# Kernel tuning notes

Hardware: AMD Instinct MI355X
Metric: run time of the kernel (lower is better)

The kernel has to match this reference:

```python
import jax, jax.numpy as jnp
import numpy as np

# Quantum kernel closed form:
#   Encoder applies RY(x_k) on wire k from |0>, then RY(-y_k); RY(-y)RY(x) = RY(x-y).
#   Amplitude of |0...0> = prod_k <0|RY(x_k - y_k)|0> = prod_k cos((x_k - y_k)/2).
#   kernel(x, y) = | prod_k cos((x_k - y_k)/2) |.
# Using cos(a-b) = cos a cos b + sin a sin b avoids forming explicit pairwise diffs twice.

def setup_inputs() -> dict:
    key = jax.random.key(0)
    x = jax.random.normal(key, (32, 1024, 4), dtype=jnp.float32)  # [B, S, n_wires]
    return {"x": x}


def reference(x) -> jnp.ndarray:
    c = jnp.cos(0.5 * x)  # [B, S, W]
    s = jnp.sin(0.5 * x)
    # cos((x_i,k - x_j,k)/2) for all pairs -> [B, S, S, W]
    term = c[:, :, None, :] * c[:, None, :, :] + s[:, :, None, :] * s[:, None, :, :]
    kernel_mat = jnp.abs(jnp.prod(term, axis=-1))  # [B, S, S]
    attn = jax.nn.softmax(kernel_mat, axis=-1)
    return jnp.matmul(attn, x)  # [B, S, W]
```

## Files before the change

### kernel.cpp

```cpp
#include <hip/hip_runtime.h>


typedef _Float16 f16x8 __attribute__((ext_vector_type(8)));
typedef float    f32x16 __attribute__((ext_vector_type(16)));
typedef unsigned int u32x4 __attribute__((ext_vector_type(4)));

#define SQ 1024
#define NTHREADS 256
#define ROWS 32

__device__ __forceinline__ unsigned pk16(float a, float b) {
    auto p = __builtin_amdgcn_cvt_pkrtz(a, b);
    return __builtin_bit_cast(unsigned, p);
}

#if __has_builtin(__builtin_amdgcn_permlane32_swap)
__device__ __forceinline__ void pl32swap(unsigned &a, unsigned &b) {
    auto r = __builtin_amdgcn_permlane32_swap(a, b, false, false);
    a = r[0]; b = r[1];
}
#else
__device__ __forceinline__ void pl32swap(unsigned &a, unsigned &b) {
    asm("v_permlane32_swap_b32 %0, %1" : "+v"(a), "+v"(b));
}
#endif

__global__ __launch_bounds__(NTHREADS, 3)
void qka_kernel(const float* __restrict__ x, float* __restrict__ out) {
    __shared__ f16x8 lds_F0[SQ];
    __shared__ f16x8 lds_F1[SQ];
    __shared__ f16x8 lds_XT[5 * 129];

    const int bid   = blockIdx.x;
    const int b     = bid >> 5;
    const int Ibase = (bid & 31) * ROWS;
    const int tid   = threadIdx.x;

    const float4* xb  = (const float4*)(x + (size_t)b * SQ * 4);
    _Float16*     xtp = (_Float16*)lds_XT;

    #pragma unroll
    for (int k = 0; k < SQ / NTHREADS; ++k) {
        int j = tid + k * NTHREADS;
        float4 v = xb[j];
        float c0 = __cosf(0.5f * v.x), s0 = __sinf(0.5f * v.x);
        float c1 = __cosf(0.5f * v.y), s1 = __sinf(0.5f * v.y);
        float c2 = __cosf(0.5f * v.z), s2 = __sinf(0.5f * v.z);
        float c3 = __cosf(0.5f * v.w), s3 = __sinf(0.5f * v.w);
        float m0 = c0 * c1, m1 = s0 * c1, m2 = c0 * s1, m3 = s0 * s1;
        float n0 = m0 * c2, n1 = m1 * c2, n2 = m2 * c2, n3 = m3 * c2;
        float n4 = m0 * s2, n5 = m1 * s2, n6 = m2 * s2, n7 = m3 * s2;
        f16x8 p0, p1;
        p0[0] = (_Float16)(n0 * c3); p0[1] = (_Float16)(n1 * c3);
        p0[2] = (_Float16)(n2 * c3); p0[3] = (_Float16)(n3 * c3);
        p0[4] = (_Float16)(n4 * c3); p0[5] = (_Float16)(n5 * c3);
        p0[6] = (_Float16)(n6 * c3); p0[7] = (_Float16)(n7 * c3);
        p1[0] = (_Float16)(n0 * s3); p1[1] = (_Float16)(n1 * s3);
        p1[2] = (_Float16)(n2 * s3); p1[3] = (_Float16)(n3 * s3);
        p1[4] = (_Float16)(n4 * s3); p1[5] = (_Float16)(n5 * s3);
        p1[6] = (_Float16)(n6 * s3); p1[7] = (_Float16)(n7 * s3);
        int sj = j ^ ((j >> 3) & 7);
        lds_F0[sj] = p0;
        lds_F1[sj] = p1;
        xtp[0 * 1032 + j] = (_Float16)v.x;
        xtp[1 * 1032 + j] = (_Float16)v.y;
        xtp[2 * 1032 + j] = (_Float16)v.z;
        xtp[3 * 1032 + j] = (_Float16)v.w;
        xtp[4 * 1032 + j] = (_Float16)1.0f;
    }
    __syncthreads();

    const int wid  = tid >> 6;
    const int lane = tid & 63;
    const int h    = lane >> 5;
    const int ln   = lane & 31;

    const f16x8* Fh = h ? lds_F1 : lds_F0;
    int ib = Ibase + ln; ib ^= (ib >> 3) & 7;
    const f16x8 bfrag = Fh[ib];

    const int rowsel = (ln < 4) ? ln : 4;
    const int xbase  = rowsel * 129 + wid * 32 + h;

    f32x16 oacc = (f32x16)(0.0f);

    #pragma unroll 2
    for (int t = 0; t < 8; ++t) {
        int ja = wid * 256 + t * 32 + ln;
        ja ^= (ja >> 3) & 7;
        f16x8 afrag = Fh[ja];
        f32x16 d = __builtin_amdgcn_mfma_f32_32x32x16_f16(
            afrag, bfrag, (f32x16)(0.0f), 0, 0, 0);
        unsigned q0 = pk16(__expf(fabsf(d[0])),  __expf(fabsf(d[1])));
        unsigned q1 = pk16(__expf(fabsf(d[2])),  __expf(fabsf(d[3])));
        unsigned q2 = pk16(__expf(fabsf(d[4])),  __expf(fabsf(d[5])));
        unsigned q3 = pk16(__expf(fabsf(d[6])),  __expf(fabsf(d[7])));
        unsigned q4 = pk16(__expf(fabsf(d[8])),  __expf(fabsf(d[9])));
        unsigned q5 = pk16(__expf(fabsf(d[10])), __expf(fabsf(d[11])));
        unsigned q6 = pk16(__expf(fabsf(d[12])), __expf(fabsf(d[13])));
        unsigned q7 = pk16(__expf(fabsf(d[14])), __expf(fabsf(d[15])));
        pl32swap(q0, q2); pl32swap(q1, q3);
        pl32swap(q4, q6); pl32swap(q5, q7);
        u32x4 w0 = {q0, q1, q2, q3};
        u32x4 w1 = {q4, q5, q6, q7};
        f16x8 ef0 = __builtin_bit_cast(f16x8, w0);
        f16x8 ef1 = __builtin_bit_cast(f16x8, w1);
        f16x8 xf0 = lds_XT[xbase + t * 4];
        f16x8 xf1 = lds_XT[xbase + t * 4 + 2];
        oacc = __builtin_amdgcn_mfma_f32_32x32x16_f16(ef0, xf0, oacc, 0, 0, 0);
        oacc = __builtin_amdgcn_mfma_f32_32x32x16_f16(ef1, xf1, oacc, 0, 0, 0);
    }

    __syncthreads();
    float* ps = (float*)lds_F0;
    if (ln < 5) {
        #pragma unroll
        for (int r = 0; r < 16; ++r) {
            int m = (r & 3) + 8 * (r >> 2) + 4 * h;
            ps[(wid * 32 + m) * 8 + ln] = oacc[r];
        }
    }
    __syncthreads();

    if (tid < 32) {
        float nx = 0.f, ny = 0.f, nz = 0.f, nw = 0.f, den = 0.f;
        #pragma unroll
        for (int ww = 0; ww < 4; ++ww) {
            const float* p = &ps[(ww * 32 + tid) * 8];
            nx += p[0]; ny += p[1]; nz += p[2]; nw += p[3]; den += p[4];
        }
        float inv = 1.0f / den;
        ((float4*)out)[(size_t)b * SQ + Ibase + tid] =
            make_float4(nx * inv, ny * inv, nz * inv, nw * inv);
    }
}

extern "C" void kernel_launch(void* const* d_in, const int* in_sizes, int n_in,
                              void* d_out, int out_size, void* d_ws, size_t ws_size,
                              hipStream_t stream) {
    const float* x = (const float*)d_in[0];
    float* out = (float*)d_out;
    dim3 grid(32 * (SQ / ROWS));
    dim3 block(NTHREADS);
    qka_kernel<<<grid, block, 0, stream>>>(x, out);
}
```

Baseline: 13.47 us.

## Double rows per block, software-pipeline score MFMA, use exp2 with prescaled features

Each block now has 512 threads and handles 64 query rows, with two row tiles sharing one LDS feature table. This halves the number of blocks and the redundant per-batch trig and LDS setup. The score MFMA for the next tile is issued before the exp/pack of the current one, and the output accumulation is split into two independent accumulators to shorten MFMA dependency chains. The exp is replaced by a raw exp2 builtin, with the log2(e) scale folded into one feature factor. This relies on |sqrt(log2 e)^2 · d| equalling |d|·log2 e, and the larger scale factor adds a little fp16 rounding.

```diff
diff --git a/kernel.cpp b/kernel.cpp
--- a/kernel.cpp
+++ b/kernel.cpp
@@ -6,8 +6,8 @@
 typedef unsigned int u32x4 __attribute__((ext_vector_type(4)));
 
 #define SQ 1024
-#define NTHREADS 256
-#define ROWS 32
+#define NTHREADS 512
+#define ROWS 64
 
 __device__ __forceinline__ unsigned pk16(float a, float b) {
     auto p = __builtin_amdgcn_cvt_pkrtz(a, b);
@@ -25,15 +25,19 @@
 }
 #endif
 
-__global__ __launch_bounds__(NTHREADS, 3)
+__device__ __forceinline__ float ex2(float v) {
+    return __builtin_amdgcn_exp2f(fabsf(v));
+}
+
+__global__ __launch_bounds__(NTHREADS, 4)
 void qka_kernel(const float* __restrict__ x, float* __restrict__ out) {
     __shared__ f16x8 lds_F0[SQ];
     __shared__ f16x8 lds_F1[SQ];
     __shared__ f16x8 lds_XT[5 * 129];
 
     const int bid   = blockIdx.x;
-    const int b     = bid >> 5;
-    const int Ibase = (bid & 31) * ROWS;
+    const int b     = bid >> 4;
+    const int Ibase = (bid & 15) * ROWS;
     const int tid   = threadIdx.x;
 
     const float4* xb  = (const float4*)(x + (size_t)b * SQ * 4);
@@ -43,10 +47,11 @@
     for (int k = 0; k < SQ / NTHREADS; ++k) {
         int j = tid + k * NTHREADS;
         float4 v = xb[j];
+        const float SC = 1.2011224087f;
         float c0 = __cosf(0.5f * v.x), s0 = __sinf(0.5f * v.x);
         float c1 = __cosf(0.5f * v.y), s1 = __sinf(0.5f * v.y);
         float c2 = __cosf(0.5f * v.z), s2 = __sinf(0.5f * v.z);
-        float c3 = __cosf(0.5f * v.w), s3 = __sinf(0.5f * v.w);
+        float c3 = SC * __cosf(0.5f * v.w), s3 = SC * __sinf(0.5f * v.w);
         float m0 = c0 * c1, m1 = s0 * c1, m2 = c0 * s1, m3 = s0 * s1;
         float n0 = m0 * c2, n1 = m1 * c2, n2 = m2 * c2, n3 = m3 * c2;
         float n4 = m0 * s2, n5 = m1 * s2, n6 = m2 * s2, n7 = m3 * s2;
@@ -71,34 +76,44 @@
     __syncthreads();
 
     const int wid  = tid >> 6;
+    const int q    = wid & 3;
+    const int rt   = wid >> 2;
     const int lane = tid & 63;
     const int h    = lane >> 5;
     const int ln   = lane & 31;
 
     const f16x8* Fh = h ? lds_F1 : lds_F0;
-    int ib = Ibase + ln; ib ^= (ib >> 3) & 7;
+    int ib = Ibase + rt * 32 + ln; ib ^= (ib >> 3) & 7;
     const f16x8 bfrag = Fh[ib];
 
     const int rowsel = (ln < 4) ? ln : 4;
-    const int xbase  = rowsel * 129 + wid * 32 + h;
+    const int xbase  = rowsel * 129 + q * 32 + h;
 
-    f32x16 oacc = (f32x16)(0.0f);
+    f32x16 oacc0 = (f32x16)(0.0f);
+    f32x16 oacc1 = (f32x16)(0.0f);
+
+    int ja = q * 256 + ln;
+    f16x8 af = Fh[ja ^ ((ja >> 3) & 7)];
+    f32x16 d = __builtin_amdgcn_mfma_f32_32x32x16_f16(
+        af, bfrag, (f32x16)(0.0f), 0, 0, 0);
 
     #pragma unroll 2
     for (int t = 0; t < 8; ++t) {
-        int ja = wid * 256 + t * 32 + ln;
-        ja ^= (ja >> 3) & 7;
-        f16x8 afrag = Fh[ja];
-        f32x16 d = __builtin_amdgcn_mfma_f32_32x32x16_f16(
-            afrag, bfrag, (f32x16)(0.0f), 0, 0, 0);
-        unsigned q0 = pk16(__expf(fabsf(d[0])),  __expf(fabsf(d[1])));
-        unsigned q1 = pk16(__expf(fabsf(d[2])),  __expf(fabsf(d[3])));
-        unsigned q2 = pk16(__expf(fabsf(d[4])),  __expf(fabsf(d[5])));
-        unsigned q3 = pk16(__expf(fabsf(d[6])),  __expf(fabsf(d[7])));
-        unsigned q4 = pk16(__expf(fabsf(d[8])),  __expf(fabsf(d[9])));
-        unsigned q5 = pk16(__expf(fabsf(d[10])), __expf(fabsf(d[11])));
-        unsigned q6 = pk16(__expf(fabsf(d[12])), __expf(fabsf(d[13])));
-        unsigned q7 = pk16(__expf(fabsf(d[14])), __expf(fabsf(d[15])));
+        f32x16 dn;
+        if (t < 7) {
+            int jn = q * 256 + (t + 1) * 32 + ln;
+            f16x8 afn = Fh[jn ^ ((jn >> 3) & 7)];
+            dn = __builtin_amdgcn_mfma_f32_32x32x16_f16(
+                afn, bfrag, (f32x16)(0.0f), 0, 0, 0);
+        }
+        unsigned q0 = pk16(ex2(d[0]),  ex2(d[1]));
+        unsigned q1 = pk16(ex2(d[2]),  ex2(d[3]));
+        unsigned q2 = pk16(ex2(d[4]),  ex2(d[5]));
+        unsigned q3 = pk16(ex2(d[6]),  ex2(d[7]));
+        unsigned q4 = pk16(ex2(d[8]),  ex2(d[9]));
+        unsigned q5 = pk16(ex2(d[10]), ex2(d[11]));
+        unsigned q6 = pk16(ex2(d[12]), ex2(d[13]));
+        unsigned q7 = pk16(ex2(d[14]), ex2(d[15]));
         pl32swap(q0, q2); pl32swap(q1, q3);
         pl32swap(q4, q6); pl32swap(q5, q7);
         u32x4 w0 = {q0, q1, q2, q3};
@@ -107,8 +122,9 @@
         f16x8 ef1 = __builtin_bit_cast(f16x8, w1);
         f16x8 xf0 = lds_XT[xbase + t * 4];
         f16x8 xf1 = lds_XT[xbase + t * 4 + 2];
-        oacc = __builtin_amdgcn_mfma_f32_32x32x16_f16(ef0, xf0, oacc, 0, 0, 0);
-        oacc = __builtin_amdgcn_mfma_f32_32x32x16_f16(ef1, xf1, oacc, 0, 0, 0);
+        oacc0 = __builtin_amdgcn_mfma_f32_32x32x16_f16(ef0, xf0, oacc0, 0, 0, 0);
+        oacc1 = __builtin_amdgcn_mfma_f32_32x32x16_f16(ef1, xf1, oacc1, 0, 0, 0);
+        if (t < 7) d = dn;
     }
 
     __syncthreads();
@@ -117,16 +133,16 @@
         #pragma unroll
         for (int r = 0; r < 16; ++r) {
             int m = (r & 3) + 8 * (r >> 2) + 4 * h;
-            ps[(wid * 32 + m) * 8 + ln] = oacc[r];
+            ps[(q * 64 + rt * 32 + m) * 8 + ln] = oacc0[r] + oacc1[r];
         }
     }
     __syncthreads();
 
-    if (tid < 32) {
+    if (tid < ROWS) {
         float nx = 0.f, ny = 0.f, nz = 0.f, nw = 0.f, den = 0.f;
         #pragma unroll
-        for (int ww = 0; ww < 4; ++ww) {
-            const float* p = &ps[(ww * 32 + tid) * 8];
+        for (int qq = 0; qq < 4; ++qq) {
+            const float* p = &ps[(qq * 64 + tid) * 8];
             nx += p[0]; ny += p[1]; nz += p[2]; nw += p[3]; den += p[4];
         }
         float inv = 1.0f / den;
```

After: 12.09 us. 1.11x faster.
